# Kernel optimization log

Measured on AMD Instinct MI355X. Metric: run time of the kernel, lower is better.

## Reference

```python
import jax, jax.numpy as jnp
import numpy as np

B, C, H, W = 4, 128, 64, 64
HEADS = 4
HD = C // HEADS
HIDDEN = 2 * C
EPS = 1e-5


def layernorm(x, w, b):
    # normalize over last axis
    mu = jnp.mean(x, axis=-1, keepdims=True)
    var = jnp.mean(jnp.square(x - mu), axis=-1, keepdims=True)
    return (x - mu) * jax.lax.rsqrt(var + EPS) * w + b


def setup_inputs() -> dict:
    key = jax.random.key(0)
    ks = jax.random.split(key, 8)
    s = 0.02
    return {
        "x": jax.random.normal(ks[0], (B, C, H, W), dtype=jnp.float32),
        "ln1_w": jnp.ones((C,), jnp.float32),
        "ln1_b": jnp.zeros((C,), jnp.float32),
        "qkv_w": jax.random.normal(ks[1], (3 * C, C), jnp.float32) * s,
        "proj_w": jax.random.normal(ks[2], (C, C), jnp.float32) * s,
        "proj_b": jnp.zeros((C,), jnp.float32),
        "ln2_w": jnp.ones((C,), jnp.float32),
        "ln2_b": jnp.zeros((C,), jnp.float32),
        "fc1_w": jax.random.normal(ks[3], (HIDDEN, C), jnp.float32) * s,
        "fc1_b": jnp.zeros((HIDDEN,), jnp.float32),
        "fc2_w": jax.random.normal(ks[4], (C, HIDDEN), jnp.float32) * s,
        "fc2_b": jnp.zeros((C,), jnp.float32),
    }


def reference(x, ln1_w, ln1_b, qkv_w, proj_w, proj_b, ln2_w, ln2_b,
              fc1_w, fc1_b, fc2_w, fc2_b):
    b, c, h, w = x.shape
    n = h * w
    # LN1 over channels (channels-last), back to NCHW
    x_ln = layernorm(jnp.transpose(x, (0, 2, 3, 1)), ln1_w, ln1_b)  # [B,H,W,C]
    # 1x1 conv qkv (no bias): einsum over channels
    qkv = jnp.einsum('bhwc,oc->bohw', x_ln, qkv_w)  # [B,3C,H,W]
    q, k, v = jnp.split(qkv, 3, axis=1)
    # [B, heads, head_dim, N]
    q = q.reshape(b, HEADS, HD, n)
    k = k.reshape(b, HEADS, HD, n)
    v = v.reshape(b, HEADS, HD, n)
    scale = 1.0 / jnp.sqrt(jnp.float32(HD))
    scores = jnp.einsum('bhdn,bhdm->bhnm', q, k) * scale  # [B,heads,N,N]
    attn = jax.nn.softmax(scores, axis=-1)
    out = jnp.einsum('bhnm,bhdm->bhdn', attn, v)  # [B,heads,head_dim,N]
    out = out.reshape(b, c, h, w)
    # 1x1 conv proj (with bias)
    out = jnp.einsum('bchw,oc->bohw', out, proj_w) + proj_b[None, :, None, None]
    x = x + out
    # LN2 + MLP
    x_ln2 = layernorm(jnp.transpose(x, (0, 2, 3, 1)), ln2_w, ln2_b)  # [B,H,W,C]
    x_flat = x_ln2.reshape(b, n, c)
    hdn = jax.nn.gelu(jnp.einsum('bnc,oc->bno', x_flat, fc1_w) + fc1_b, approximate=False)
    x_mlp = jnp.einsum('bno,co->bnc', hdn, fc2_w) + fc2_b
    x_mlp = jnp.transpose(x_mlp.reshape(b, h, w, c), (0, 3, 1, 2))
    return x + x_mlp
```

## Files before the change

### kernel.cpp

```cpp
#include <hip/hip_runtime.h>
#include <hip/hip_bf16.h>


typedef __attribute__((ext_vector_type(4))) float f32x4;
typedef __attribute__((ext_vector_type(8))) short bf16x8;
typedef __attribute__((ext_vector_type(8))) unsigned short ushort8;
typedef __attribute__((ext_vector_type(4))) unsigned short ushort4v;

#define C_ 128
#define N_ 4096
#define SL2E 0.25504712280087033f
#define EXP2R(x) __builtin_amdgcn_exp2f(x)

__device__ inline unsigned short f2bf(float f) {
  unsigned int x = __float_as_uint(f);
  x += 0x7fffu + ((x >> 16) & 1u);
  return (unsigned short)(x >> 16);
}

__device__ inline unsigned int pk2(float a, float b) {
  __hip_bfloat162 h2 = __float22bfloat162_rn(make_float2(a, b));
  return *(unsigned int*)&h2;
}

__global__ __launch_bounds__(256) void wconv_kernel(const float* __restrict__ qkvw,
                                                    const float* __restrict__ projw,
                                                    const float* __restrict__ fc1w,
                                                    const float* __restrict__ fc2w,
                                                    unsigned short* __restrict__ WB) {
  int i = blockIdx.x * 256 + threadIdx.x;
  float v;
  if (i < 49152) v = qkvw[i];
  else if (i < 65536) v = projw[i - 49152];
  else if (i < 98304) v = fc1w[i - 65536];
  else v = fc2w[i - 98304];
  WB[i] = f2bf(v);
}

__global__ __launch_bounds__(256) void ln_kernel(const float* __restrict__ xin,
                                                 const float* __restrict__ gamma,
                                                 const float* __restrict__ beta,
                                                 unsigned short* __restrict__ outp) {
  __shared__ float tile[128][33];
  __shared__ float ps[8][32];
  __shared__ float pss[8][32];
  __shared__ float mu_s[32];
  __shared__ float rs_s[32];
  const int t = threadIdx.x;
  const int b = blockIdx.x >> 7;
  const int n0 = (blockIdx.x & 127) << 5;
  const float* xb = xin + (size_t)b * C_ * N_ + n0;
#pragma unroll
  for (int i = 0; i < 16; ++i) {
    int lin = i * 256 + t;
    int c = lin >> 5, p = lin & 31;
    tile[c][p] = xb[(size_t)c * N_ + p];
  }
  __syncthreads();
  {
    int p = t & 31, part = t >> 5;
    float s = 0.f, ss = 0.f;
#pragma unroll
    for (int j = 0; j < 16; ++j) {
      float v = tile[part * 16 + j][p];
      s += v; ss += v * v;
    }
    ps[part][p] = s; pss[part][p] = ss;
  }
  __syncthreads();
  if (t < 32) {
    float su = 0.f, sq = 0.f;
#pragma unroll
    for (int k = 0; k < 8; ++k) { su += ps[k][t]; sq += pss[k][t]; }
    float mu = su * (1.f / 128.f);
    float var = sq * (1.f / 128.f) - mu * mu;
    mu_s[t] = mu;
    rs_s[t] = rsqrtf(var + 1e-5f);
  }
  __syncthreads();
  unsigned short* ob = outp + (size_t)(b * N_ + n0) * C_;
#pragma unroll
  for (int i = 0; i < 8; ++i) {
    int lin = i * 256 + t;
    int p = lin >> 6, c2 = (lin & 63) << 1;
    float mu = mu_s[p], rs = rs_s[p];
    float a = (tile[c2][p] - mu) * rs * gamma[c2] + beta[c2];
    float d = (tile[c2 + 1][p] - mu) * rs * gamma[c2 + 1] + beta[c2 + 1];
    *(unsigned int*)&ob[(size_t)p * C_ + c2] = pk2(a, d);
  }
}

template <int KD>
__device__ inline void mfma_core(const unsigned short* __restrict__ A,
                                 const unsigned short* __restrict__ W,
                                 int row0, int col0, f32x4 acc[2][4]) {
  __shared__ __align__(16) unsigned short As[128][128];
  __shared__ __align__(16) unsigned short Ws[64][128];
  const int t = threadIdx.x;
  const int w = t >> 6, lane = t & 63;
  const int l15 = lane & 15, g = lane >> 4;
  const int srow = t >> 4, schunk = t & 15;
#pragma unroll
  for (int kt = 0; kt < KD / 128; ++kt) {
    __syncthreads();
#pragma unroll
    for (int i = 0; i < 8; ++i) {
      int row = i * 16 + srow;
      int c = schunk ^ (row & 7);
      *(ushort8*)&As[row][c * 8] =
          *(const ushort8*)&A[(size_t)(row0 + row) * KD + kt * 128 + schunk * 8];
    }
#pragma unroll
    for (int i = 0; i < 4; ++i) {
      int row = i * 16 + srow;
      int c = schunk ^ (row & 7);
      *(ushort8*)&Ws[row][c * 8] =
          *(const ushort8*)&W[(size_t)(col0 + row) * KD + kt * 128 + schunk * 8];
    }
    __syncthreads();
#pragma unroll
    for (int kk = 0; kk < 4; ++kk) {
      bf16x8 aA[2], bW[4];
#pragma unroll
      for (int mi = 0; mi < 2; ++mi) {
        int mrow = (w << 5) + (mi << 4) + l15;
        int c = (kk * 4 + g) ^ (mrow & 7);
        aA[mi] = *(const bf16x8*)&As[mrow][c * 8];
      }
#pragma unroll
      for (int nj = 0; nj < 4; ++nj) {
        int wrow = (nj << 4) + l15;
        int c = (kk * 4 + g) ^ (wrow & 7);
        bW[nj] = *(const bf16x8*)&Ws[wrow][c * 8];
      }
#pragma unroll
      for (int mi = 0; mi < 2; ++mi)
#pragma unroll
        for (int nj = 0; nj < 4; ++nj)
          acc[mi][nj] = __builtin_amdgcn_mfma_f32_16x16x32_bf16(aA[mi], bW[nj],
                                                                acc[mi][nj], 0, 0, 0);
    }
  }
}

__global__ __launch_bounds__(256) void qkv_kernel(const unsigned short* __restrict__ XLN,
                                                  const unsigned short* __restrict__ Wq,
                                                  unsigned short* __restrict__ Qb,
                                                  unsigned short* __restrict__ Kb,
                                                  unsigned short* __restrict__ Vb) {
  const int row0 = blockIdx.x << 7, col0 = blockIdx.y << 6;
  f32x4 acc[2][4] = {};
  mfma_core<128>(XLN, Wq, row0, col0, acc);
  const int t = threadIdx.x, w = t >> 6, lane = t & 63;
  const int l15 = lane & 15, g = lane >> 4;
#pragma unroll
  for (int mi = 0; mi < 2; ++mi) {
    int grow = row0 + (w << 5) + (mi << 4) + (g << 2);
    int b = grow >> 12, n0 = grow & 4095;
#pragma unroll
    for (int nj = 0; nj < 4; ++nj) {
      int o = col0 + (nj << 4) + l15;
      int ch = o & 127, hh = ch >> 5, d = ch & 31;
      f32x4 a = acc[mi][nj];
      if (o < 128) {
        size_t base = ((size_t)(b * 4 + hh) * 4096 + n0) * 32 + d;
#pragma unroll
        for (int r = 0; r < 4; ++r) Qb[base + (size_t)r * 32] = f2bf(a[r] * SL2E);
      } else if (o < 256) {
        size_t base = ((size_t)(b * 4 + hh) * 4096 + n0) * 32 + d;
#pragma unroll
        for (int r = 0; r < 4; ++r) Kb[base + (size_t)r * 32] = f2bf(a[r]);
      } else {
        ushort4v u = {f2bf(a[0]), f2bf(a[1]), f2bf(a[2]), f2bf(a[3])};
        *(ushort4v*)&Vb[((size_t)(b * 4 + hh) * 32 + d) * 4096 + n0] = u;
      }
    }
  }
}

#define ATTN_CHUNK(CUR, KT)                                                     \
  {                                                                             \
    if ((KT) < 63) {                                                            \
      kreg = *(const ushort8*)kp_n;  kp_n += 64 * 32;                           \
      vreg = *(const ushort8*)vp_n;  vp_n += 64;                                \
    }                                                                           \
    f32x4 s[4];                                                                 \
    _Pragma("unroll")                                                           \
    for (int ks = 0; ks < 4; ++ks) {                                            \
      bf16x8 bK = *(const bf16x8*)&Ks[CUR][(ks << 4) + l15][g << 3];            \
      s[ks] = __builtin_amdgcn_mfma_f32_16x16x32_bf16(bK, aQ, cneg, 0, 0, 0);   \
    }                                                                           \
    float a0 = fmaxf(fmaxf(s[0][0], s[0][1]), s[0][2]);                         \
    float a1 = fmaxf(fmaxf(s[0][3], s[1][0]), s[1][1]);                         \
    float a2 = fmaxf(fmaxf(s[1][2], s[1][3]), s[2][0]);                         \
    float a3 = fmaxf(fmaxf(s[2][1], s[2][2]), s[2][3]);                         \
    float a4 = fmaxf(fmaxf(s[3][0], s[3][1]), s[3][2]);                         \
    float m0 = fmaxf(fmaxf(fmaxf(a0, a1), fmaxf(a2, a3)), fmaxf(a4, s[3][3]));  \
    float p[4][4];                                                              \
    if (__builtin_expect(!__all(m0 <= 8.f), 0)) {                               \
      m0 = fmaxf(m0, __shfl_xor(m0, 16));                                       \
      m0 = fmaxf(m0, __shfl_xor(m0, 32));                                       \
      float d = fmaxf(m0, 0.f);                                                 \
      float al = EXP2R(-d);                                                     \
      m_r += d;                                                                 \
      cneg = zero - m_r;                                                        \
      opv[0] *= al;  opv[1] *= al;  lsum *= al;                                 \
      _Pragma("unroll")                                                         \
      for (int ks = 0; ks < 4; ++ks)                                            \
        _Pragma("unroll")                                                       \
        for (int r = 0; r < 4; ++r) p[ks][r] = EXP2R(s[ks][r] - d);             \
    } else {                                                                    \
      _Pragma("unroll")                                                         \
      for (int ks = 0; ks < 4; ++ks)                                            \
        _Pragma("unroll")                                                       \
        for (int r = 0; r < 4; ++r) p[ks][r] = EXP2R(s[ks][r]);                 \
    }                                                                           \
    _Pragma("unroll")                                                           \
    for (int pi = 0; pi < 2; ++pi) {                                            \
      union { unsigned int u[4]; bf16x8 v; } bP;                                \
      bP.u[0] = pk2(p[2 * pi][0], p[2 * pi][1]);                                \
      bP.u[1] = pk2(p[2 * pi][2], p[2 * pi][3]);                                \
      bP.u[2] = pk2(p[2 * pi + 1][0], p[2 * pi + 1][1]);                        \
      bP.u[3] = pk2(p[2 * pi + 1][2], p[2 * pi + 1][3]);                        \
      lsum = __builtin_amdgcn_mfma_f32_16x16x32_bf16(ones, bP.v, lsum, 0, 0, 0);\
      _Pragma("unroll")                                                         \
      for (int dt = 0; dt < 2; ++dt) {                                          \
        bf16x8 aV =                                                             \
            *(const bf16x8*)&Vt[CUR][(dt << 4) + l15][(pi << 5) + (g << 3)];    \
        opv[dt] = __builtin_amdgcn_mfma_f32_16x16x32_bf16(aV, bP.v, opv[dt],    \
                                                          0, 0, 0);             \
      }                                                                         \
    }                                                                           \
    if ((KT) < 63) {                                                            \
      *(ushort8*)&Ks[(CUR) ^ 1][krow][kd0] = kreg;                              \
      ushort4v lo = {vreg[0], vreg[1], vreg[2], vreg[3]};                       \
      ushort4v hi = {vreg[4], vreg[5], vreg[6], vreg[7]};                       \
      *(ushort4v*)&Vt[(CUR) ^ 1][vd][vpos] = lo;                                \
      *(ushort4v*)&Vt[(CUR) ^ 1][vd][vpos + 8] = hi;                            \
    }                                                                           \
    __syncthreads();                                                            \
  }

__global__ __launch_bounds__(256) void attn_kernel(const unsigned short* __restrict__ Qg,
                                                   const unsigned short* __restrict__ Kg,
                                                   const unsigned short* __restrict__ Vg,
                                                   unsigned short* __restrict__ AO) {
  __shared__ __align__(16) unsigned short Qa[64][40];
  __shared__ __align__(16) unsigned short Ks[2][64][40];
  __shared__ __align__(16) unsigned short Vt[2][32][72];
  const int id = blockIdx.x;
  const int bh = (id & 7) | ((id >> 9) << 3);
  const int qt = (id >> 3) & 63;
  const int b = bh >> 2, h = bh & 3;
  const unsigned short* Qp = Qg + ((size_t)bh * 4096 + qt * 64) * 32;
  const unsigned short* Kp = Kg + (size_t)bh * 4096 * 32;
  const unsigned short* Vp = Vg + (size_t)bh * 32 * 4096;
  const int t = threadIdx.x;
  const int lane = t & 63, w = t >> 6;
  const int l15 = lane & 15, g = lane >> 4;
  const int krow = t >> 2, kd0 = (t & 3) << 3;
  const int vd = t >> 3, vc = t & 7;
  const int vpos = ((vc >> 2) << 5) + ((vc & 1) << 4) + (((vc & 3) >> 1) << 2);

  *(ushort8*)&Qa[krow][kd0] = *(const ushort8*)(Qp + krow * 32 + kd0);
  ushort8 kreg = *(const ushort8*)(Kp + (size_t)krow * 32 + kd0);
  ushort8 vreg = *(const ushort8*)(Vp + (size_t)vd * 4096 + (vc << 3));
  const unsigned short* kp_n = Kp + 64 * 32 + (size_t)krow * 32 + kd0;
  const unsigned short* vp_n = Vp + (size_t)vd * 4096 + 64 + (vc << 3);
  *(ushort8*)&Ks[0][krow][kd0] = kreg;
  {
    ushort4v lo = {vreg[0], vreg[1], vreg[2], vreg[3]};
    ushort4v hi = {vreg[4], vreg[5], vreg[6], vreg[7]};
    *(ushort4v*)&Vt[0][vd][vpos] = lo;
    *(ushort4v*)&Vt[0][vd][vpos + 8] = hi;
  }
  __syncthreads();
  const bf16x8 aQ = *(const bf16x8*)&Qa[(w << 4) + l15][g << 3];
  const short oneb = (short)0x3F80;
  const bf16x8 ones = {oneb, oneb, oneb, oneb, oneb, oneb, oneb, oneb};

  const f32x4 zero = {0.f, 0.f, 0.f, 0.f};
  f32x4 opv[2]; opv[0] = zero; opv[1] = zero;
  f32x4 lsum = zero;
  f32x4 cneg = zero;
  float m_r = 0.f;

  for (int kt2 = 0; kt2 < 64; kt2 += 2) {
    ATTN_CHUNK(0, kt2);
    ATTN_CHUNK(1, kt2 + 1);
  }

  float inv = 1.f / lsum[0];
  const int n = qt * 64 + (w << 4) + l15;
  unsigned short* aob = AO + (size_t)(b * 4096 + n) * 128 + (h << 5);
#pragma unroll
  for (int dt = 0; dt < 2; ++dt) {
    f32x4 o = opv[dt] * inv;
    ushort4v u = {f2bf(o[0]), f2bf(o[1]), f2bf(o[2]), f2bf(o[3])};
    *(ushort4v*)&aob[(dt << 4) + (g << 2)] = u;
  }
}

__global__ __launch_bounds__(256) void proj_kernel(const unsigned short* __restrict__ AO,
                                                   const unsigned short* __restrict__ Wp,
                                                   const float* __restrict__ bp,
                                                   const float* __restrict__ x,
                                                   float* __restrict__ X1) {
  const int row0 = blockIdx.x << 7, col0 = blockIdx.y << 6;
  f32x4 acc[2][4] = {};
  mfma_core<128>(AO, Wp, row0, col0, acc);
  const int t = threadIdx.x, w = t >> 6, lane = t & 63;
  const int l15 = lane & 15, g = lane >> 4;
#pragma unroll
  for (int mi = 0; mi < 2; ++mi) {
    int grow = row0 + (w << 5) + (mi << 4) + (g << 2);
    int b = grow >> 12, n0 = grow & 4095;
#pragma unroll
    for (int nj = 0; nj < 4; ++nj) {
      int c = col0 + (nj << 4) + l15;
      size_t idx = ((size_t)(b * C_ + c) << 12) + n0;
      f32x4 xv = *(const f32x4*)&x[idx];
      f32x4 r = xv + acc[mi][nj] + bp[c];
      *(f32x4*)&X1[idx] = r;
    }
  }
}

__global__ __launch_bounds__(256) void fc1_kernel(const unsigned short* __restrict__ XLN2,
                                                  const unsigned short* __restrict__ W1,
                                                  const float* __restrict__ b1,
                                                  unsigned short* __restrict__ Hb) {
  const int row0 = blockIdx.x << 7, col0 = blockIdx.y << 6;
  f32x4 acc[2][4] = {};
  mfma_core<128>(XLN2, W1, row0, col0, acc);
  const int t = threadIdx.x, w = t >> 6, lane = t & 63;
  const int l15 = lane & 15, g = lane >> 4;
#pragma unroll
  for (int mi = 0; mi < 2; ++mi) {
    int grow = row0 + (w << 5) + (mi << 4) + (g << 2);
#pragma unroll
    for (int nj = 0; nj < 4; ++nj) {
      int o = col0 + (nj << 4) + l15;
      float bb = b1[o];
#pragma unroll
      for (int r = 0; r < 4; ++r) {
        float v = acc[mi][nj][r] + bb;
        v = 0.5f * v * (1.f + erff(v * 0.70710678118654752f));
        Hb[(size_t)(grow + r) * 256 + o] = f2bf(v);
      }
    }
  }
}

__global__ __launch_bounds__(256) void fc2_kernel(const unsigned short* __restrict__ Hb,
                                                  const unsigned short* __restrict__ W2,
                                                  const float* __restrict__ b2,
                                                  const float* __restrict__ X1,
                                                  float* __restrict__ outp) {
  const int row0 = blockIdx.x << 7, col0 = blockIdx.y << 6;
  f32x4 acc[2][4] = {};
  mfma_core<256>(Hb, W2, row0, col0, acc);
  const int t = threadIdx.x, w = t >> 6, lane = t & 63;
  const int l15 = lane & 15, g = lane >> 4;
#pragma unroll
  for (int mi = 0; mi < 2; ++mi) {
    int grow = row0 + (w << 5) + (mi << 4) + (g << 2);
    int b = grow >> 12, n0 = grow & 4095;
#pragma unroll
    for (int nj = 0; nj < 4; ++nj) {
      int c = col0 + (nj << 4) + l15;
      size_t idx = ((size_t)(b * C_ + c) << 12) + n0;
      f32x4 xv = *(const f32x4*)&X1[idx];
      f32x4 r = xv + acc[mi][nj] + b2[c];
      *(f32x4*)&outp[idx] = r;
    }
  }
}

extern "C" void kernel_launch(void* const* d_in, const int* in_sizes, int n_in,
                              void* d_out, int out_size, void* d_ws, size_t ws_size,
                              hipStream_t stream) {
  (void)in_sizes; (void)n_in; (void)out_size; (void)ws_size;
  const float* x     = (const float*)d_in[0];
  const float* ln1w  = (const float*)d_in[1];
  const float* ln1b  = (const float*)d_in[2];
  const float* qkvw  = (const float*)d_in[3];
  const float* projw = (const float*)d_in[4];
  const float* projb = (const float*)d_in[5];
  const float* ln2w  = (const float*)d_in[6];
  const float* ln2b  = (const float*)d_in[7];
  const float* fc1w  = (const float*)d_in[8];
  const float* fc1b  = (const float*)d_in[9];
  const float* fc2w  = (const float*)d_in[10];
  const float* fc2b  = (const float*)d_in[11];
  float* out = (float*)d_out;
  char* ws8 = (char*)d_ws;

  const size_t MB = 1u << 20;
  unsigned short* WB   = (unsigned short*)(ws8);
  unsigned short* XLN  = (unsigned short*)(ws8 + 1 * MB);
  unsigned short* Qb   = (unsigned short*)(ws8 + 5 * MB);
  unsigned short* Kb   = (unsigned short*)(ws8 + 9 * MB);
  unsigned short* Vb   = (unsigned short*)(ws8 + 13 * MB);
  unsigned short* AObf = XLN;
  unsigned short* XLN2 = Qb;
  unsigned short* HB   = Kb;
  float*          X1   = (float*)(ws8 + 17 * MB);
  const unsigned short* Wqkv = WB;
  const unsigned short* Wproj = WB + 49152;
  const unsigned short* Wfc1 = WB + 65536;
  const unsigned short* Wfc2 = WB + 98304;

  wconv_kernel<<<dim3(512), dim3(256), 0, stream>>>(qkvw, projw, fc1w, fc2w, WB);
  ln_kernel<<<dim3(512), dim3(256), 0, stream>>>(x, ln1w, ln1b, XLN);
  qkv_kernel<<<dim3(128, 6), dim3(256), 0, stream>>>(XLN, Wqkv, Qb, Kb, Vb);
  attn_kernel<<<dim3(1024), dim3(256), 0, stream>>>(Qb, Kb, Vb, AObf);
  proj_kernel<<<dim3(128, 2), dim3(256), 0, stream>>>(AObf, Wproj, projb, x, X1);
  ln_kernel<<<dim3(512), dim3(256), 0, stream>>>(X1, ln2w, ln2b, XLN2);
  fc1_kernel<<<dim3(128, 4), dim3(256), 0, stream>>>(XLN2, Wfc1, fc1b, HB);
  fc2_kernel<<<dim3(128, 2), dim3(256), 0, stream>>>(HB, Wfc2, fc2b, X1, out);
}
```

Before: 197.6 us.

## Fuse projection GEMM with residual add and LayerNorm2 into one kernel

Replaces the separate proj and LN2 kernels with one kernel. Each block computes a full 64-row by 128-channel projection tile via MFMA from swizzled shared memory, adds the residual and bias, then does the per-row LayerNorm with cross-lane shuffles and writes bf16 XLN2. This removes one launch and the re-read of X1 from global memory. In exchange it has fewer blocks (256) and uses single-pass variance. The pk2 helper also now uses an inline v_cvt_pk_bf16_f32 instruction.

```diff
diff --git a/kernel.cpp b/kernel.cpp
--- a/kernel.cpp
+++ b/kernel.cpp
@@ -19,8 +19,9 @@
 }
 
 __device__ inline unsigned int pk2(float a, float b) {
-  __hip_bfloat162 h2 = __float22bfloat162_rn(make_float2(a, b));
-  return *(unsigned int*)&h2;
+  unsigned int r;
+  asm("v_cvt_pk_bf16_f32 %0, %1, %2" : "=v"(r) : "v"(a), "v"(b));
+  return r;
 }
 
 __global__ __launch_bounds__(256) void wconv_kernel(const float* __restrict__ qkvw,
@@ -301,27 +302,94 @@
   }
 }
 
-__global__ __launch_bounds__(256) void proj_kernel(const unsigned short* __restrict__ AO,
-                                                   const unsigned short* __restrict__ Wp,
-                                                   const float* __restrict__ bp,
-                                                   const float* __restrict__ x,
-                                                   float* __restrict__ X1) {
-  const int row0 = blockIdx.x << 7, col0 = blockIdx.y << 6;
-  f32x4 acc[2][4] = {};
-  mfma_core<128>(AO, Wp, row0, col0, acc);
-  const int t = threadIdx.x, w = t >> 6, lane = t & 63;
-  const int l15 = lane & 15, g = lane >> 4;
-#pragma unroll
-  for (int mi = 0; mi < 2; ++mi) {
-    int grow = row0 + (w << 5) + (mi << 4) + (g << 2);
-    int b = grow >> 12, n0 = grow & 4095;
-#pragma unroll
-    for (int nj = 0; nj < 4; ++nj) {
-      int c = col0 + (nj << 4) + l15;
-      size_t idx = ((size_t)(b * C_ + c) << 12) + n0;
-      f32x4 xv = *(const f32x4*)&x[idx];
-      f32x4 r = xv + acc[mi][nj] + bp[c];
-      *(f32x4*)&X1[idx] = r;
+__global__ __launch_bounds__(256) void proj_ln2_kernel(
+    const unsigned short* __restrict__ AO,
+    const unsigned short* __restrict__ Wp,
+    const float* __restrict__ bp,
+    const float* __restrict__ x,
+    const float* __restrict__ g2,
+    const float* __restrict__ b2,
+    float* __restrict__ X1,
+    unsigned short* __restrict__ XLN2) {
+  __shared__ __align__(16) unsigned short As[64][128];
+  __shared__ __align__(16) unsigned short Ws[128][128];
+  const int t = threadIdx.x;
+  const int w = t >> 6, lane = t & 63;
+  const int l15 = lane & 15, g = lane >> 4;
+  const int srow = t >> 4, schunk = t & 15;
+  const int row0 = blockIdx.x << 6;
+#pragma unroll
+  for (int i = 0; i < 4; ++i) {
+    int row = i * 16 + srow;
+    int c = schunk ^ (row & 7);
+    *(ushort8*)&As[row][c * 8] =
+        *(const ushort8*)&AO[(size_t)(row0 + row) * 128 + schunk * 8];
+  }
+#pragma unroll
+  for (int i = 0; i < 8; ++i) {
+    int row = i * 16 + srow;
+    int c = schunk ^ (row & 7);
+    *(ushort8*)&Ws[row][c * 8] =
+        *(const ushort8*)&Wp[(size_t)row * 128 + schunk * 8];
+  }
+  __syncthreads();
+  f32x4 acc[8];
+#pragma unroll
+  for (int nj = 0; nj < 8; ++nj) acc[nj] = (f32x4){0.f, 0.f, 0.f, 0.f};
+#pragma unroll
+  for (int kk = 0; kk < 4; ++kk) {
+    int mrow = (w << 4) + l15;
+    int ca = (kk * 4 + g) ^ (mrow & 7);
+    bf16x8 aA = *(const bf16x8*)&As[mrow][ca * 8];
+#pragma unroll
+    for (int nj = 0; nj < 8; ++nj) {
+      int wrow = (nj << 4) + l15;
+      int cw = (kk * 4 + g) ^ (wrow & 7);
+      bf16x8 bW = *(const bf16x8*)&Ws[wrow][cw * 8];
+      acc[nj] = __builtin_amdgcn_mfma_f32_16x16x32_bf16(aA, bW, acc[nj], 0, 0, 0);
+    }
+  }
+  const int grow = row0 + (w << 4) + (g << 2);
+  const int b = grow >> 12, n0 = grow & 4095;
+  f32x4 val[8];
+  f32x4 s = {0.f, 0.f, 0.f, 0.f}, ss = {0.f, 0.f, 0.f, 0.f};
+#pragma unroll
+  for (int nj = 0; nj < 8; ++nj) {
+    int c = (nj << 4) + l15;
+    size_t idx = ((size_t)(b * C_ + c) << 12) + n0;
+    f32x4 xv = *(const f32x4*)&x[idx];
+    val[nj] = xv + acc[nj] + bp[c];
+    *(f32x4*)&X1[idx] = val[nj];
+    s += val[nj];
+    ss += val[nj] * val[nj];
+  }
+#pragma unroll
+  for (int m = 1; m < 16; m <<= 1) {
+    f32x4 so, sso;
+#pragma unroll
+    for (int r = 0; r < 4; ++r) {
+      so[r] = __shfl_xor(s[r], m, 16);
+      sso[r] = __shfl_xor(ss[r], m, 16);
+    }
+    s += so;
+    ss += sso;
+  }
+  f32x4 mu = s * (1.f / 128.f);
+  f32x4 rs;
+#pragma unroll
+  for (int r = 0; r < 4; ++r) {
+    float var = ss[r] * (1.f / 128.f) - mu[r] * mu[r];
+    rs[r] = rsqrtf(var + 1e-5f);
+  }
+  unsigned short* ob = XLN2 + (size_t)grow * C_;
+#pragma unroll
+  for (int nj = 0; nj < 8; ++nj) {
+    int c = (nj << 4) + l15;
+    float gam = g2[c], bet = b2[c];
+#pragma unroll
+    for (int r = 0; r < 4; ++r) {
+      float v = (val[nj][r] - mu[r]) * rs[r] * gam + bet;
+      ob[(size_t)r * C_ + c] = f2bf(v);
     }
   }
 }
@@ -415,8 +483,8 @@
   ln_kernel<<<dim3(512), dim3(256), 0, stream>>>(x, ln1w, ln1b, XLN);
   qkv_kernel<<<dim3(128, 6), dim3(256), 0, stream>>>(XLN, Wqkv, Qb, Kb, Vb);
   attn_kernel<<<dim3(1024), dim3(256), 0, stream>>>(Qb, Kb, Vb, AObf);
-  proj_kernel<<<dim3(128, 2), dim3(256), 0, stream>>>(AObf, Wproj, projb, x, X1);
-  ln_kernel<<<dim3(512), dim3(256), 0, stream>>>(X1, ln2w, ln2b, XLN2);
+  proj_ln2_kernel<<<dim3(256), dim3(256), 0, stream>>>(AObf, Wproj, projb, x,
+                                                       ln2w, ln2b, X1, XLN2);
   fc1_kernel<<<dim3(128, 4), dim3(256), 0, stream>>>(XLN2, Wfc1, fc1b, HB);
   fc2_kernel<<<dim3(128, 2), dim3(256), 0, stream>>>(HB, Wfc2, fc2b, X1, out);
 }
```

Result: faster. 185.5 us (-6.1%).
